# Optimization experiments

Hardware: AMD Instinct MI355X
Metric: run time of the kernel (lower is better)

The kernel has to match this reference:

```python
import jax, jax.numpy as jnp
import numpy as np

E, K = 8, 2          # n_experts, top-k
D, O = 768, 3072     # input_size, output_size
B, S = 4, 512        # batch, seq


def setup_inputs() -> dict:
    key = jax.random.key(0)
    k1, k2, k3, k4, k5 = jax.random.split(key, 5)
    x = jax.random.normal(k1, (B, S, D), jnp.float32)
    w_gate = jax.random.normal(k2, (D, E), jnp.float32) * 0.02
    expert_w = jax.random.normal(k3, (E, O, D), jnp.float32) * 0.02
    expert_b = jax.random.normal(k4, (E, O), jnp.float32) * 0.02
    static_w = jax.random.normal(k5, (O, D), jnp.float32) * 0.02
    return {"x": x, "w_gate": w_gate, "expert_w": expert_w,
            "expert_b": expert_b, "static_w": static_w}


def cv_squared(v):
    # torch .var() is unbiased (ddof=1)
    return jnp.var(v, ddof=1) / (jnp.mean(v) ** 2 + 1e-10)


def reference(x, w_gate, expert_w, expert_b, static_w):
    loss_coef = 0.01
    xf = x.reshape(-1, D)                      # [N, D]
    N = xf.shape[0]

    # --- top-k gating (eval path: no noise) ---
    logits = xf @ w_gate                       # [N, E]
    top_v, top_i = jax.lax.top_k(logits, K + 1)
    top_k_gates = jax.nn.softmax(top_v[:, :K], axis=1)   # [N, K]
    gates = jnp.zeros_like(logits).at[
        jnp.arange(N)[:, None], top_i[:, :K]].set(top_k_gates)  # [N, E]

    importance = gates.sum(0)                  # [E]
    load = (gates > 0).sum(0).astype(jnp.float32)
    loss = (cv_squared(importance) + cv_squared(load)) * loss_coef

    # --- experts: F.linear(h, W_e + static_w, b_e), combined by gates ---
    W = expert_w + static_w[None]              # [E, O, D]
    y_e = jnp.einsum('nd,eod->neo', xf, W) + expert_b[None]   # [N, E, O]
    y = jnp.einsum('neo,ne->no', y_e, gates)   # [N, O]

    return y.reshape(B, S, O), loss
```

## Files before the change

kernel.cpp:

```cpp
#include <hip/hip_runtime.h>
#include <hip/hip_bf16.h>
#include <stdint.h>

#define E_ 8
#define K_ 2
#define D_ 768
#define O_ 3072
#define N_ 2048

typedef __attribute__((ext_vector_type(8))) __bf16 bf16x8;
typedef __attribute__((ext_vector_type(4))) float f32x4;

__device__ __forceinline__ unsigned short f2bf(float f) {
    union { float f; uint32_t u; } a; a.f = f;
    uint32_t u = a.u;
    uint32_t r = (u + 0x7fffu + ((u >> 16) & 1u)) >> 16;
    return (unsigned short)r;
}

__device__ __forceinline__ void async16(const void* g, void* l) {
    __builtin_amdgcn_global_load_lds(
        (const __attribute__((address_space(1))) void*)g,
        (__attribute__((address_space(3))) void*)l, 16, 0, 0);
}

__global__ __launch_bounds__(256) void gating_kernel(
    const float* __restrict__ x, const float* __restrict__ w_gate,
    unsigned short* __restrict__ xb, int* __restrict__ choice_e,
    float* __restrict__ choice_g, float* __restrict__ y)
{
    int wid  = threadIdx.x >> 6;
    int lane = threadIdx.x & 63;
    int n = blockIdx.x * 4 + wid;
    const float* xr = x + (size_t)n * D_;

    float acc[E_];
#pragma unroll
    for (int e = 0; e < E_; ++e) acc[e] = 0.f;

    for (int c = 0; c < D_ / 64; ++c) {
        int d = c * 64 + lane;
        float xv = xr[d];
        xb[(size_t)n * D_ + d] = f2bf(xv);
        const float* wg = w_gate + (size_t)d * E_;
        float4 w0 = *(const float4*)(wg);
        float4 w1 = *(const float4*)(wg + 4);
        acc[0] += xv * w0.x; acc[1] += xv * w0.y;
        acc[2] += xv * w0.z; acc[3] += xv * w0.w;
        acc[4] += xv * w1.x; acc[5] += xv * w1.y;
        acc[6] += xv * w1.z; acc[7] += xv * w1.w;
    }
#pragma unroll
    for (int e = 0; e < E_; ++e) {
        float v = acc[e];
        for (int off = 32; off > 0; off >>= 1) v += __shfl_xor(v, off, 64);
        acc[e] = v;
    }
    if (lane == 0) {
        int i0 = 0; float v0 = acc[0];
#pragma unroll
        for (int e = 1; e < E_; ++e) if (acc[e] > v0) { v0 = acc[e]; i0 = e; }
        int i1 = -1; float v1 = -3.0e38f;
#pragma unroll
        for (int e = 0; e < E_; ++e) if (e != i0 && acc[e] > v1) { v1 = acc[e]; i1 = e; }
        float ex = expf(v1 - v0);
        float g0 = 1.f / (1.f + ex);
        float g1 = ex / (1.f + ex);
        choice_e[2 * n]     = i0;  choice_g[2 * n]     = g0;
        choice_e[2 * n + 1] = i1;  choice_g[2 * n + 1] = g1;
    }

    float4 z = {0.f, 0.f, 0.f, 0.f};
    float4* yb = (float4*)(y + (size_t)blockIdx.x * 12288);
#pragma unroll
    for (int i = 0; i < 12; ++i) yb[threadIdx.x + 256 * i] = z;
}

__global__ __launch_bounds__(1024) void compact_kernel(
    const int* __restrict__ choice_e, const float* __restrict__ choice_g,
    int* __restrict__ counts, int* __restrict__ pair_token,
    float* __restrict__ pair_gate, float* __restrict__ out_loss)
{
    __shared__ int   s_cnt[E_];
    __shared__ float s_imp[E_];
    int t = threadIdx.x;
    if (t < E_) { s_cnt[t] = 0; s_imp[t] = 0.f; }
    __syncthreads();
    for (int i = t; i < N_ * 2; i += 1024) {
        int e = choice_e[i];
        float gv = choice_g[i];
        int pos = atomicAdd(&s_cnt[e], 1);
        pair_token[e * N_ + pos] = i >> 1;
        pair_gate[e * N_ + pos]  = gv;
        atomicAdd(&s_imp[e], gv);
    }
    __syncthreads();
    if (t < E_) counts[t] = s_cnt[t];
    if (t == 0) {
        float mi = 0.f, ml = 0.f, imp[E_], ld[E_];
#pragma unroll
        for (int i = 0; i < E_; ++i) {
            imp[i] = s_imp[i]; ld[i] = (float)s_cnt[i];
            mi += imp[i]; ml += ld[i];
        }
        mi /= (float)E_; ml /= (float)E_;
        float vi = 0.f, vl = 0.f;
#pragma unroll
        for (int i = 0; i < E_; ++i) {
            vi += (imp[i] - mi) * (imp[i] - mi);
            vl += (ld[i] - ml) * (ld[i] - ml);
        }
        vi /= (float)(E_ - 1); vl /= (float)(E_ - 1);
        *out_loss = 0.01f * (vi / (mi * mi + 1e-10f) + vl / (ml * ml + 1e-10f));
    }
}

__global__ __launch_bounds__(256) void prep_w_kernel(
    const float* __restrict__ ew, const float* __restrict__ sw,
    unsigned short* __restrict__ wb)
{
    int i = blockIdx.x * 256 + threadIdx.x;
    int f = i * 4;
    const int od = O_ * D_;
    int e = f / od;
    int rem = f - e * od;
    float4 a = *(const float4*)(ew + f);
    float4 b = *(const float4*)(sw + rem);
    ushort4 o;
    o.x = f2bf(a.x + b.x); o.y = f2bf(a.y + b.y);
    o.z = f2bf(a.z + b.z); o.w = f2bf(a.w + b.w);
    ((ushort4*)wb)[i] = o;
}

#define BM 128
#define BN 128
#define BK 64

__global__ __launch_bounds__(256) void moe_gemm_kernel(
    const unsigned short* __restrict__ xb,
    const unsigned short* __restrict__ wb,
    const float* __restrict__ expert_b,
    const int* __restrict__ counts,
    const int* __restrict__ pair_token,
    const float* __restrict__ pair_gate,
    float* __restrict__ y)
{
    int e = blockIdx.z;
    int cnt = counts[e];
    int m0 = blockIdx.y * BM;
    if (m0 >= cnt) return;
    int n0 = blockIdx.x * BN;

    __shared__ __align__(16) unsigned short sA[(BK / 8) * BM * 8];
    __shared__ __align__(16) unsigned short sB[(BK / 8) * BN * 8];

    int tid  = threadIdx.x;
    int lane = tid & 63;
    int wid  = tid >> 6;
    int wm = wid & 1, wn = wid >> 1;
    int l16 = lane & 15;
    int quad = lane >> 4;

    int srow = tid & 127;
    int kchb = tid >> 7;
    int arow = m0 + srow; if (arow >= cnt) arow = cnt - 1;
    int stok = pair_token[e * N_ + arow];
    const unsigned short* ga = xb + (size_t)stok * D_;
    const unsigned short* gb = wb + ((size_t)e * O_ + n0 + srow) * D_;
    char* sAb = (char*)sA + wid * 1024;
    char* sBb = (char*)sB + wid * 1024;

    f32x4 acc[4][4];
#pragma unroll
    for (int a = 0; a < 4; ++a)
#pragma unroll
        for (int b = 0; b < 4; ++b) acc[a][b] = (f32x4){0.f, 0.f, 0.f, 0.f};

    for (int k0 = 0; k0 < D_; k0 += BK) {
#pragma unroll
        for (int s = 0; s < 4; ++s) {
            int kch = kchb + 2 * s;
            async16(ga + k0 + kch * 8, sAb + s * 4096);
            async16(gb + k0 + kch * 8, sBb + s * 4096);
        }
        __syncthreads();

#pragma unroll
        for (int ks = 0; ks < 2; ++ks) {
            int kch = ks * 4 + quad;
            bf16x8 af[4], bfr[4];
#pragma unroll
            for (int mi = 0; mi < 4; ++mi)
                af[mi] = *(const bf16x8*)&sA[(kch * BM + wm * 64 + mi * 16 + l16) * 8];
#pragma unroll
            for (int ni = 0; ni < 4; ++ni)
                bfr[ni] = *(const bf16x8*)&sB[(kch * BN + wn * 64 + ni * 16 + l16) * 8];
#pragma unroll
            for (int mi = 0; mi < 4; ++mi)
#pragma unroll
                for (int ni = 0; ni < 4; ++ni)
                    acc[mi][ni] = __builtin_amdgcn_mfma_f32_16x16x32_bf16(
                        af[mi], bfr[ni], acc[mi][ni], 0, 0, 0);
        }
        __syncthreads();
    }

    float bias[4];
#pragma unroll
    for (int ni = 0; ni < 4; ++ni)
        bias[ni] = expert_b[e * O_ + n0 + wn * 64 + ni * 16 + l16];
#pragma unroll
    for (int mi = 0; mi < 4; ++mi) {
        int rb = m0 + wm * 64 + mi * 16 + quad * 4;
#pragma unroll
        for (int reg = 0; reg < 4; ++reg) {
            int r = rb + reg;
            if (r < cnt) {
                int token  = pair_token[e * N_ + r];
                float gate = pair_gate[e * N_ + r];
#pragma unroll
                for (int ni = 0; ni < 4; ++ni) {
                    int o = n0 + wn * 64 + ni * 16 + l16;
                    atomicAdd(&y[(size_t)token * O_ + o],
                              gate * (acc[mi][ni][reg] + bias[ni]));
                }
            }
        }
    }
}

extern "C" void kernel_launch(void* const* d_in, const int* in_sizes, int n_in,
                              void* d_out, int out_size, void* d_ws, size_t ws_size,
                              hipStream_t stream) {
    const float* x        = (const float*)d_in[0];
    const float* w_gate   = (const float*)d_in[1];
    const float* expert_w = (const float*)d_in[2];
    const float* expert_b = (const float*)d_in[3];
    const float* static_w = (const float*)d_in[4];
    float* out = (float*)d_out;

    char* ws = (char*)d_ws;
    int*   counts     = (int*)(ws + 0);
    int*   pair_token = (int*)(ws + 4096);
    float* pair_gate  = (float*)(ws + 4096 + 65536);
    int*   choice_e   = (int*)(ws + 4096 + 131072);
    float* choice_g   = (float*)(ws + 4096 + 131072 + 16384);
    unsigned short* xb = (unsigned short*)(ws + 4096 + 131072 + 32768);
    unsigned short* wb = (unsigned short*)(ws + 4096 + 131072 + 32768 + 3145728);

    gating_kernel<<<N_ / 4, 256, 0, stream>>>(x, w_gate, xb, choice_e, choice_g, out);
    compact_kernel<<<1, 1024, 0, stream>>>(choice_e, choice_g, counts,
                                           pair_token, pair_gate, out + (size_t)N_ * O_);
    prep_w_kernel<<<(E_ * O_ * D_ / 4) / 256, 256, 0, stream>>>(expert_w, static_w, wb);

    dim3 grid(O_ / BN, N_ / BM, E_);
    moe_gemm_kernel<<<grid, 256, 0, stream>>>(xb, wb, expert_b, counts,
                                              pair_token, pair_gate, out);
}
```

Measured before the change: 234.6 us.

## Merge gating and weight prep kernels; switch GEMM LDS tiles to XOR-swizzled row-major

Gating and the expert-weight bf16 conversion now run in one launch, with block index deciding which job a block does. This removes a kernel launch and lets the two memory-bound jobs share the GPU. The GEMM's shared-memory layout changes from k-chunk-major to row-major with an XOR swizzle on the 16-byte k chunk. Each thread now loads a contiguous 128-byte row segment from global memory, which gives better coalescing, while the swizzle is meant to avoid LDS bank conflicts on the fragment reads. The risk is that the async LDS-load destination mapping must stay consistent with the swizzled read indexing.

```diff
diff --git a/kernel.cpp b/kernel.cpp
--- a/kernel.cpp
+++ b/kernel.cpp
@@ -3,7 +3,6 @@
 #include <stdint.h>
 
 #define E_ 8
-#define K_ 2
 #define D_ 768
 #define O_ 3072
 #define N_ 2048
@@ -24,11 +23,28 @@
         (__attribute__((address_space(3))) void*)l, 16, 0, 0);
 }
 
-__global__ __launch_bounds__(256) void gating_kernel(
+__global__ __launch_bounds__(256) void prologue_kernel(
     const float* __restrict__ x, const float* __restrict__ w_gate,
-    unsigned short* __restrict__ xb, int* __restrict__ choice_e,
-    float* __restrict__ choice_g, float* __restrict__ y)
+    const float* __restrict__ ew, const float* __restrict__ sw,
+    unsigned short* __restrict__ xb, unsigned short* __restrict__ wb,
+    int* __restrict__ choice_e, float* __restrict__ choice_g,
+    float* __restrict__ y)
 {
+    if (blockIdx.x >= 512) {
+        int i = (blockIdx.x - 512) * 256 + threadIdx.x;
+        int f = i * 4;
+        const int od = O_ * D_;
+        int e = f / od;
+        int rem = f - e * od;
+        float4 a = *(const float4*)(ew + f);
+        float4 b = *(const float4*)(sw + rem);
+        ushort4 o;
+        o.x = f2bf(a.x + b.x); o.y = f2bf(a.y + b.y);
+        o.z = f2bf(a.z + b.z); o.w = f2bf(a.w + b.w);
+        ((ushort4*)wb)[i] = o;
+        return;
+    }
+
     int wid  = threadIdx.x >> 6;
     int lane = threadIdx.x & 63;
     int n = blockIdx.x * 4 + wid;
@@ -115,23 +131,6 @@
     }
 }
 
-__global__ __launch_bounds__(256) void prep_w_kernel(
-    const float* __restrict__ ew, const float* __restrict__ sw,
-    unsigned short* __restrict__ wb)
-{
-    int i = blockIdx.x * 256 + threadIdx.x;
-    int f = i * 4;
-    const int od = O_ * D_;
-    int e = f / od;
-    int rem = f - e * od;
-    float4 a = *(const float4*)(ew + f);
-    float4 b = *(const float4*)(sw + rem);
-    ushort4 o;
-    o.x = f2bf(a.x + b.x); o.y = f2bf(a.y + b.y);
-    o.z = f2bf(a.z + b.z); o.w = f2bf(a.w + b.w);
-    ((ushort4*)wb)[i] = o;
-}
-
 #define BM 128
 #define BN 128
 #define BK 64
@@ -151,8 +150,8 @@
     if (m0 >= cnt) return;
     int n0 = blockIdx.x * BN;
 
-    __shared__ __align__(16) unsigned short sA[(BK / 8) * BM * 8];
-    __shared__ __align__(16) unsigned short sB[(BK / 8) * BN * 8];
+    __shared__ __align__(16) unsigned short sA[BM * BK];
+    __shared__ __align__(16) unsigned short sB[BN * BK];
 
     int tid  = threadIdx.x;
     int lane = tid & 63;
@@ -161,14 +160,19 @@
     int l16 = lane & 15;
     int quad = lane >> 4;
 
-    int srow = tid & 127;
-    int kchb = tid >> 7;
-    int arow = m0 + srow; if (arow >= cnt) arow = cnt - 1;
-    int stok = pair_token[e * N_ + arow];
-    const unsigned short* ga = xb + (size_t)stok * D_;
-    const unsigned short* gb = wb + ((size_t)e * O_ + n0 + srow) * D_;
-    char* sAb = (char*)sA + wid * 1024;
-    char* sBb = (char*)sB + wid * 1024;
+    int r0 = tid >> 3;
+    int kg = (tid & 7) ^ (r0 & 7);
+    const unsigned short* gA[4];
+    const unsigned short* gB[4];
+#pragma unroll
+    for (int s = 0; s < 4; ++s) {
+        int row = r0 + 32 * s;
+        int ar = m0 + row; if (ar >= cnt) ar = cnt - 1;
+        gA[s] = xb + (size_t)pair_token[e * N_ + ar] * D_ + kg * 8;
+        gB[s] = wb + ((size_t)e * O_ + n0 + row) * D_ + kg * 8;
+    }
+    char* lA = (char*)sA + wid * 1024;
+    char* lB = (char*)sB + wid * 1024;
 
     f32x4 acc[4][4];
 #pragma unroll
@@ -179,22 +183,26 @@
     for (int k0 = 0; k0 < D_; k0 += BK) {
 #pragma unroll
         for (int s = 0; s < 4; ++s) {
-            int kch = kchb + 2 * s;
-            async16(ga + k0 + kch * 8, sAb + s * 4096);
-            async16(gb + k0 + kch * 8, sBb + s * 4096);
+            async16(gA[s] + k0, lA + s * 4096);
+            async16(gB[s] + k0, lB + s * 4096);
         }
         __syncthreads();
 
 #pragma unroll
         for (int ks = 0; ks < 2; ++ks) {
-            int kch = ks * 4 + quad;
             bf16x8 af[4], bfr[4];
 #pragma unroll
-            for (int mi = 0; mi < 4; ++mi)
-                af[mi] = *(const bf16x8*)&sA[(kch * BM + wm * 64 + mi * 16 + l16) * 8];
-#pragma unroll
-            for (int ni = 0; ni < 4; ++ni)
-                bfr[ni] = *(const bf16x8*)&sB[(kch * BN + wn * 64 + ni * 16 + l16) * 8];
+            for (int mi = 0; mi < 4; ++mi) {
+                int row = wm * 64 + mi * 16 + l16;
+                int ch  = row * 8 + ((ks * 4 + quad) ^ (row & 7));
+                af[mi] = *(const bf16x8*)&sA[ch * 8];
+            }
+#pragma unroll
+            for (int ni = 0; ni < 4; ++ni) {
+                int row = wn * 64 + ni * 16 + l16;
+                int ch  = row * 8 + ((ks * 4 + quad) ^ (row & 7));
+                bfr[ni] = *(const bf16x8*)&sB[ch * 8];
+            }
 #pragma unroll
             for (int mi = 0; mi < 4; ++mi)
 #pragma unroll
@@ -248,10 +256,10 @@
     unsigned short* xb = (unsigned short*)(ws + 4096 + 131072 + 32768);
     unsigned short* wb = (unsigned short*)(ws + 4096 + 131072 + 32768 + 3145728);
 
-    gating_kernel<<<N_ / 4, 256, 0, stream>>>(x, w_gate, xb, choice_e, choice_g, out);
+    prologue_kernel<<<512 + (E_ * O_ * D_ / 4) / 256, 256, 0, stream>>>(
+        x, w_gate, expert_w, static_w, xb, wb, choice_e, choice_g, out);
     compact_kernel<<<1, 1024, 0, stream>>>(choice_e, choice_g, counts,
                                            pair_token, pair_gate, out + (size_t)N_ * O_);
-    prep_w_kernel<<<(E_ * O_ * D_ / 4) / 256, 256, 0, stream>>>(expert_w, static_w, wb);
 
     dim3 grid(O_ / BN, N_ / BM, E_);
     moe_gemm_kernel<<<grid, 256, 0, stream>>>(xb, wb, expert_b, counts,
```

New measurement: 210.2 us. -10.4%, faster.
